# Kernel optimization log

Measured on AMD Instinct MI355X. Metric: run time of the kernel, lower is better.

The kernel has to match this reference:

```python
import jax, jax.numpy as jnp
import numpy as np

B, S, E = 4, 2048, 512
H, D = 8, 64
MIN_W, MAX_W = 256, 1024
EPS = 1e-6


def setup_inputs() -> dict:
    key = jax.random.key(0)
    ks = jax.random.split(key, 9)
    w = lambda k, shp: jax.random.normal(k, shp, dtype=jnp.float32) * 0.02
    return {
        "x": jax.random.normal(ks[0], (B, S, E), dtype=jnp.float32),
        "rms1_w": jnp.ones((E,), jnp.float32),
        "rms2_w": jnp.ones((E,), jnp.float32),
        "qkv_w": w(ks[1], (3 * E, E)),
        "out_w": w(ks[2], (E, E)),
        "cs_w1": w(ks[3], (E // 4, E)),
        "cs_w2": w(ks[4], (1, E // 4)),
        "gate_w": w(ks[5], (2304, E)),
        "up_w": w(ks[6], (2304, E)),
        "down_w": w(ks[7], (E, 2304)),
    }


def _rmsnorm(x, w):
    rms = jax.lax.rsqrt(jnp.mean(x * x, axis=-1, keepdims=True) + EPS)
    return x * rms * w


def _rotate_half(x):
    x1 = x[..., ::2]
    x2 = x[..., 1::2]
    return jnp.stack((-x2, x1), axis=-1).reshape(x.shape)


def reference(x, rms1_w, rms2_w, qkv_w, out_w, cs_w1, cs_w2, gate_w, up_w, down_w):
    # --- pre-norm ---
    h = _rmsnorm(x, rms1_w)                                  # [B,S,E]
    # --- qkv ---
    qkv = h @ qkv_w.T                                        # [B,S,3E]
    qkv = qkv.reshape(B, S, 3, H, D).transpose(2, 0, 3, 1, 4)
    q, k, v = qkv[0], qkv[1], qkv[2]                         # [B,H,S,D]
    # --- RoPE (cat-freqs cos/sin + interleaved rotate_half, as in source) ---
    inv_freq = 1.0 / (10000.0 ** (jnp.arange(0, D, 2, dtype=jnp.float32) / D))
    pos = jnp.arange(S, dtype=jnp.float32)
    freqs = jnp.outer(pos, inv_freq)                         # [S,D/2]
    emb = jnp.concatenate([freqs, freqs], axis=-1)           # [S,D]
    cos = jnp.cos(emb)[None, None]
    sin = jnp.sin(emb)[None, None]
    q = q * cos + _rotate_half(q) * sin
    k = k * cos + _rotate_half(k) * sin
    # --- attention scores ---
    scale = D ** -0.5
    scores = jnp.einsum("bhqd,bhkd->bhqk", q, k) * scale     # [B,H,S,S]
    # --- complexity -> dynamic window size ---
    n = S * E
    mu = jnp.mean(h, axis=(1, 2), keepdims=True)
    var = jnp.sum((h - mu) ** 2, axis=(1, 2)) / (n - 1)      # unbiased, per batch
    var_norm = jax.nn.sigmoid(var * 10.0 - 5.0)
    xm = jnp.mean(h, axis=1)                                 # [B,E]
    learned = jax.nn.sigmoid((jax.nn.silu(xm @ cs_w1.T)) @ cs_w2.T)[:, 0]
    complexity = (var_norm + learned) / 2.0                  # [B]
    ws_f = MIN_W + jnp.mean(complexity) * (MAX_W - MIN_W)
    ws = ws_f.astype(jnp.int32)                              # trunc, like .int()
    ws = jnp.maximum(jnp.minimum(ws, S), MIN_W)
    # --- causal + sliding-window mask ---
    p = jnp.arange(S)
    rel = p[:, None] - p[None, :]                            # [S,S]
    allowed = (rel >= 0) & (rel < ws)
    scores = jnp.where(allowed[None, None], scores, -jnp.inf)
    attn = jax.nn.softmax(scores, axis=-1)
    out = jnp.einsum("bhqk,bhkd->bhqd", attn, v)             # [B,H,S,D]
    out = out.transpose(0, 2, 1, 3).reshape(B, S, E)
    out = out @ out_w.T
    x = x + out
    # --- SwiGLU FFN ---
    h2 = _rmsnorm(x, rms2_w)
    ffn = (jax.nn.silu(h2 @ gate_w.T) * (h2 @ up_w.T)) @ down_w.T
    return x + ffn
```

## Files before the change

### kernel.cpp

```cpp
#include <hip/hip_runtime.h>

typedef unsigned short u16;
typedef unsigned int   u32;
typedef __attribute__((ext_vector_type(4))) float  f32x4;
typedef __attribute__((ext_vector_type(8))) __bf16 bf16x8;
typedef __attribute__((ext_vector_type(4))) u32    u32x4;
typedef __attribute__((ext_vector_type(2))) u32    u32x2;

#define B_ 4
#define S_ 2048
#define E_ 512
#define H_ 8
#define D_ 64

__device__ __forceinline__ u16 f2bf(float f) {
  union { float f; u32 u; } a; a.f = f;
  u32 r = a.u + 0x7FFFu + ((a.u >> 16) & 1u);
  return (u16)(r >> 16);
}
__device__ __forceinline__ float bf2f(u16 u) {
  union { u32 u; float f; } a; a.u = (u32)u << 16;
  return a.f;
}
__device__ __forceinline__ u32 pkbf(float lo, float hi) {
  u32 r;
  asm("v_cvt_pk_bf16_f32 %0, %1, %2" : "=v"(r) : "v"(lo), "v"(hi));
  return r;
}

#define GLOAD16(gp, lp) __builtin_amdgcn_global_load_lds( \
    (const __attribute__((address_space(1))) void*)(gp),  \
    (__attribute__((address_space(3))) void*)(lp), 16, 0, 0)

#define BARRIER() asm volatile("s_barrier" ::: "memory")

__global__ __launch_bounds__(256) void prep_k(const float* __restrict__ qkv_w,
                                              const float* __restrict__ out_w,
                                              const float* __restrict__ gate_w,
                                              const float* __restrict__ up_w,
                                              const float* __restrict__ down_w,
                                              u16* __restrict__ wqkv, u16* __restrict__ wout,
                                              u16* __restrict__ wgate, u16* __restrict__ wup,
                                              u16* __restrict__ wdown,
                                              float* __restrict__ ct, float* __restrict__ st) {
  int bid = (int)blockIdx.x;
  const float* s; u16* d; int base;
  if (bid < 768)       { s = qkv_w;  d = wqkv;  base = bid; }
  else if (bid < 1024) { s = out_w;  d = wout;  base = bid - 768; }
  else if (bid < 2176) { s = gate_w; d = wgate; base = bid - 1024; }
  else if (bid < 3328) { s = up_w;   d = wup;   base = bid - 2176; }
  else if (bid < 4480) { s = down_w; d = wdown; base = bid - 3328; }
  else {
    int idx = (bid - 4480) * 256 + threadIdx.x;
    int sp = idx >> 6, j = idx & 63;
    float f = powf(10000.f, -(float)(j & 31) * (1.f / 32.f));
    float ang = (float)sp * f;
    ct[idx] = cosf(ang);
    st[idx] = sinf(ang);
    return;
  }
  int i = (base * 256 + threadIdx.x) * 4;
  f32x4 v = *(const f32x4*)(s + i);
  u32x2 o;
  o.x = pkbf(v[0], v[1]);
  o.y = pkbf(v[2], v[3]);
  *(u32x2*)(d + i) = o;
}

__global__ __launch_bounds__(256) void rmsnorm_k(const float* __restrict__ x,
                                                 const float* __restrict__ wv,
                                                 u16* __restrict__ o) {
  const int row = blockIdx.x;
  const int t = threadIdx.x;
  const float* xr = x + (size_t)row * E_;
  float v0 = xr[t], v1 = xr[t + 256];
  float ss = v0 * v0 + v1 * v1;
#pragma unroll
  for (int m = 1; m < 64; m <<= 1) ss += __shfl_xor(ss, m, 64);
  __shared__ float red[4];
  if ((t & 63) == 0) red[t >> 6] = ss;
  __syncthreads();
  float tot = red[0] + red[1] + red[2] + red[3];
  float rms = 1.f / sqrtf(tot * (1.f / (float)E_) + 1e-6f);
  o[(size_t)row * E_ + t]       = f2bf(v0 * rms * wv[t]);
  o[(size_t)row * E_ + t + 256] = f2bf(v1 * rms * wv[t + 256]);
}

__global__ __launch_bounds__(256) void colsum_k(const u16* __restrict__ h,
                                                float* __restrict__ st) {
  const int b = blockIdx.x >> 3, ck = blockIdx.x & 7;
  const u16* hb = h + ((size_t)b * S_ + ck * 256) * E_;
  const int t = threadIdx.x;
  float a0 = 0, a1 = 0, s = 0, sq = 0;
  for (int r = 0; r < 256; ++r) {
    float v0 = bf2f(hb[(size_t)r * E_ + t]);
    float v1 = bf2f(hb[(size_t)r * E_ + t + 256]);
    a0 += v0; a1 += v1;
    s += v0 + v1; sq += v0 * v0 + v1 * v1;
  }
  atomicAdd(&st[8 + b * E_ + t], a0);
  atomicAdd(&st[8 + b * E_ + t + 256], a1);
#pragma unroll
  for (int m = 1; m < 64; m <<= 1) { s += __shfl_xor(s, m, 64); sq += __shfl_xor(sq, m, 64); }
  if ((t & 63) == 0) { atomicAdd(&st[b], s); atomicAdd(&st[4 + b], sq); }
}

__global__ __launch_bounds__(128) void wscalc_k(float* __restrict__ st,
                                                const float* __restrict__ w1,
                                                const float* __restrict__ w2) {
  const int j = threadIdx.x;
  __shared__ float comp[4];
  __shared__ float tw[2];
  float dot[4] = {0.f, 0.f, 0.f, 0.f};
  const float* w1r = w1 + (size_t)j * E_;
  for (int e = 0; e < E_; ++e) {
    float wv = w1r[e];
    dot[0] += st[8 + 0 * E_ + e] * wv;
    dot[1] += st[8 + 1 * E_ + e] * wv;
    dot[2] += st[8 + 2 * E_ + e] * wv;
    dot[3] += st[8 + 3 * E_ + e] * wv;
  }
  for (int b = 0; b < 4; ++b) {
    float d = dot[b] * (1.f / (float)S_);
    float si = d / (1.f + __expf(-d));
    float term = si * w2[j];
#pragma unroll
    for (int m = 1; m < 64; m <<= 1) term += __shfl_xor(term, m, 64);
    __syncthreads();
    if ((j & 63) == 0) tw[j >> 6] = term;
    __syncthreads();
    if (j == 0) {
      float pre = tw[0] + tw[1];
      float learned = 1.f / (1.f + __expf(-pre));
      const float n = (float)S_ * (float)E_;
      float sum = st[b], ssq = st[4 + b];
      float var = (ssq - sum * sum / n) / (n - 1.f);
      float vn = 1.f / (1.f + __expf(-(var * 10.f - 5.f)));
      comp[b] = 0.5f * (vn + learned);
    }
    __syncthreads();
  }
  if (j == 0) {
    float mean = 0.25f * (comp[0] + comp[1] + comp[2] + comp[3]);
    float wsf = 256.f + mean * 768.f;
    int v = (int)wsf;
    v = v < 256 ? 256 : (v > S_ ? S_ : v);
    ((int*)st)[2056] = v;
  }
}

struct EpiArgs {
  u16* q; u16* k; u16* vt;
  const float* cosT; const float* sinT;
  const float* resid; float* outf;
};

template <int N, int K, int EPI>
__global__ __launch_bounds__(512) void gemm_k(const u16* __restrict__ A,
                                              const u16* __restrict__ W,
                                              EpiArgs ea) {
  constexpr int NBN = N / 128;
  __shared__ u16 sA[2][128 * 64];
  __shared__ u16 sB[2][128 * 64];
  const int tid = threadIdx.x;
  const int nwg = (int)gridDim.x;
  const int bid = (int)blockIdx.x;
  const int logical = (bid & 7) * (nwg >> 3) + (bid >> 3);
  const int bm = logical / NBN, bn = logical % NBN;
  const int lane = tid & 63, w = tid >> 6;
  const int g = lane >> 4, c = lane & 15;
  const int wrow = (w >> 1) * 32;
  const int wcol = (w & 1) * 64;

  const int lr0 = lane >> 3;
  const int scol = ((lane & 7) ^ lr0) * 8;
  const u16* gA = A + (size_t)(bm * 128 + w * 16 + lr0) * K + scol;
  const u16* gB = W + (size_t)(bn * 128 + w * 16 + lr0) * K + scol;

  f32x4 acc[2][4];
  f32x4 zz = {0.f, 0.f, 0.f, 0.f};
#pragma unroll
  for (int i = 0; i < 2; ++i)
#pragma unroll
    for (int j = 0; j < 4; ++j) acc[i][j] = zz;

  auto stage = [&](int buf, int ko) {
    GLOAD16(gA + ko,                (char*)sA[buf] + (w * 16) * 128);
    GLOAD16(gA + (size_t)8 * K + ko, (char*)sA[buf] + (w * 16 + 8) * 128);
    GLOAD16(gB + ko,                (char*)sB[buf] + (w * 16) * 128);
    GLOAD16(gB + (size_t)8 * K + ko, (char*)sB[buf] + (w * 16 + 8) * 128);
  };

  constexpr int NIT = K / 64;
  stage(0, 0);
  int cur = 0;
  for (int it = 0; it < NIT; ++it) {
    if (it + 1 < NIT) {
      stage(cur ^ 1, (it + 1) * 64);
      asm volatile("s_waitcnt vmcnt(4)" ::: "memory");
    } else {
      asm volatile("s_waitcnt vmcnt(0)" ::: "memory");
    }
    BARRIER();
    const u16* bufA = sA[cur];
    const u16* bufB = sB[cur];
    bf16x8 af[2][2], bfr[4][2];
#pragma unroll
    for (int mi = 0; mi < 2; ++mi) {
      int ar = wrow + mi * 16 + c;
#pragma unroll
      for (int kk = 0; kk < 2; ++kk)
        af[mi][kk] = *(const bf16x8*)&bufA[ar * 64 + (((kk * 4 + g) ^ (ar & 7)) * 8)];
    }
#pragma unroll
    for (int nj = 0; nj < 4; ++nj) {
      int br = wcol + nj * 16 + c;
#pragma unroll
      for (int kk = 0; kk < 2; ++kk)
        bfr[nj][kk] = *(const bf16x8*)&bufB[br * 64 + (((kk * 4 + g) ^ (br & 7)) * 8)];
    }
#pragma unroll
    for (int kk = 0; kk < 2; ++kk)
#pragma unroll
      for (int mi = 0; mi < 2; ++mi)
#pragma unroll
        for (int nj = 0; nj < 4; ++nj)
          acc[mi][nj] = __builtin_amdgcn_mfma_f32_16x16x32_bf16(af[mi][kk], bfr[nj][kk], acc[mi][nj], 0, 0, 0);
    BARRIER();
    cur ^= 1;
  }

#pragma unroll
  for (int mi = 0; mi < 2; ++mi) {
#pragma unroll
    for (int nj = 0; nj < 4; ++nj) {
      const int rowb = bm * 128 + wrow + mi * 16 + 4 * g;
      const int cc = bn * 128 + wcol + nj * 16 + c;
      if constexpr (EPI == 0) {
        const int which = cc >> 9;
        const int hh = (cc >> 6) & 7;
        const int d = cc & 63;
        const int bi = rowb >> 11;
        const int s = rowb & (S_ - 1);
        if (which == 2) {
          u32x2 pk;
          pk.x = pkbf(acc[mi][nj][0], acc[mi][nj][1]);
          pk.y = pkbf(acc[mi][nj][2], acc[mi][nj][3]);
          *(u32x2*)(ea.vt + (((size_t)(bi * H_ + hh) * D_ + d) * S_ + s)) = pk;
        } else {
          u16* dst = (which == 0 ? ea.q : ea.k) + (((size_t)(bi * H_ + hh) * S_ + s) * D_ + d);
#pragma unroll
          for (int r = 0; r < 4; ++r) {
            float v = acc[mi][nj][r];
            float pv = __shfl_xor(v, 1, 64);
            int si = s + r;
            float cs = ea.cosT[si * 64 + d];
            float sn = ea.sinT[si * 64 + d];
            float o = v * cs + ((d & 1) ? pv : -pv) * sn;
            dst[(size_t)r * D_] = f2bf(o);
          }
        }
      } else {
#pragma unroll
        for (int r = 0; r < 4; ++r) {
          size_t idx = (size_t)(rowb + r) * N + cc;
          ea.outf[idx] = acc[mi][nj][r] + ea.resid[idx];
        }
      }
    }
  }
}

__global__ __launch_bounds__(512) void gemmgu_k(const u16* __restrict__ A,
                                                const u16* __restrict__ Wg,
                                                const u16* __restrict__ Wu,
                                                u16* __restrict__ outb) {
  __shared__ u16 sA[2][128 * 32];
  __shared__ u16 sG[2][128 * 32];
  __shared__ u16 sU[2][128 * 32];
  const int tid = threadIdx.x;
  const int nwg = (int)gridDim.x;
  const int bid = (int)blockIdx.x;
  const int logical = (bid & 7) * (nwg >> 3) + (bid >> 3);
  const int bm = logical / 18, bn = logical % 18;
  const int lane = tid & 63, w = tid >> 6;
  const int g = lane >> 4, c = lane & 15;
  const int wrow = (w >> 1) * 32;
  const int wcol = (w & 1) * 64;

  const int sr0 = w * 16 + (lane >> 2);
  const int ch0 = (lane & 3) ^ ((sr0 >> 1) & 3);
  const u16* gA = A + (size_t)(bm * 128 + sr0) * 512 + ch0 * 8;
  const u16* gG = Wg + (size_t)(bn * 128 + sr0) * 512 + ch0 * 8;
  const u16* gU = Wu + (size_t)(bn * 128 + sr0) * 512 + ch0 * 8;
  const int lofs = w * 1024;

  f32x4 accg[2][4], accu[2][4];
  f32x4 zz = {0.f, 0.f, 0.f, 0.f};
#pragma unroll
  for (int i = 0; i < 2; ++i)
#pragma unroll
    for (int j = 0; j < 4; ++j) { accg[i][j] = zz; accu[i][j] = zz; }

  auto stage = [&](int buf, int ko) {
    GLOAD16(gA + ko, (char*)sA[buf] + lofs);
    GLOAD16(gG + ko, (char*)sG[buf] + lofs);
    GLOAD16(gU + ko, (char*)sU[buf] + lofs);
  };

  stage(0, 0);
  int cur = 0;
  for (int it = 0; it < 16; ++it) {
    if (it + 1 < 16) {
      stage(cur ^ 1, (it + 1) * 32);
      asm volatile("s_waitcnt vmcnt(3)" ::: "memory");
    } else {
      asm volatile("s_waitcnt vmcnt(0)" ::: "memory");
    }
    BARRIER();
    const u16* bufA = sA[cur];
    const u16* bufG = sG[cur];
    const u16* bufU = sU[cur];
    bf16x8 af[2], bg[4], bu[4];
#pragma unroll
    for (int mi = 0; mi < 2; ++mi) {
      int ar = wrow + mi * 16 + c;
      af[mi] = *(const bf16x8*)&bufA[ar * 32 + ((g ^ ((ar >> 1) & 3)) * 8)];
    }
#pragma unroll
    for (int nj = 0; nj < 4; ++nj) {
      int br = wcol + nj * 16 + c;
      int sw = (g ^ ((br >> 1) & 3)) * 8;
      bg[nj] = *(const bf16x8*)&bufG[br * 32 + sw];
      bu[nj] = *(const bf16x8*)&bufU[br * 32 + sw];
    }
#pragma unroll
    for (int mi = 0; mi < 2; ++mi)
#pragma unroll
      for (int nj = 0; nj < 4; ++nj) {
        accg[mi][nj] = __builtin_amdgcn_mfma_f32_16x16x32_bf16(af[mi], bg[nj], accg[mi][nj], 0, 0, 0);
        accu[mi][nj] = __builtin_amdgcn_mfma_f32_16x16x32_bf16(af[mi], bu[nj], accu[mi][nj], 0, 0, 0);
      }
    BARRIER();
    cur ^= 1;
  }

#pragma unroll
  for (int mi = 0; mi < 2; ++mi) {
#pragma unroll
    for (int nj = 0; nj < 4; ++nj) {
      const int rowb = bm * 128 + wrow + mi * 16 + 4 * g;
      const int cc = bn * 128 + wcol + nj * 16 + c;
#pragma unroll
      for (int r = 0; r < 4; ++r) {
        float gv = accg[mi][nj][r];
        float uv = accu[mi][nj][r];
        float sil = gv / (1.f + __expf(-gv));
        outb[(size_t)(rowb + r) * 2304 + cc] = f2bf(sil * uv);
      }
    }
  }
}

__global__ __launch_bounds__(256) void attn_k(const u16* __restrict__ Qb,
                                              const u16* __restrict__ Kb,
                                              const u16* __restrict__ Vt,
                                              u16* __restrict__ ao,
                                              const int* __restrict__ wsp) {
  __shared__ u16 sK[2][64 * 64];
  __shared__ u16 sV[2][64 * 64];
  const int bid = (int)blockIdx.x;
  const int qt = 31 - (bid >> 5);
  const int bh = bid & 31;
  const int b = bh >> 3, h = bh & 7;
  const int tid = threadIdx.x;
  const int w = tid >> 6, lane = tid & 63;
  const int g = lane >> 4, c = lane & 15;
  const int ws = *wsp;
  const int qw = qt * 64 + w * 16;
  const u16* Qh = Qb + (size_t)bh * S_ * D_;
  const u16* Kh = Kb + (size_t)bh * S_ * D_;
  const u16* Vh = Vt + (size_t)bh * D_ * S_;

  bf16x8 qf0 = *(const bf16x8*)(Qh + (qw + c) * D_ + g * 8);
  bf16x8 qf1 = *(const bf16x8*)(Qh + (qw + c) * D_ + 32 + g * 8);

  const int lr0 = lane >> 3;
  const int scol = ((lane & 7) ^ lr0) * 8;
  const u16* gK = Kh + (size_t)(w * 16 + lr0) * D_ + scol;
  const u16* gV = Vh + (size_t)(w * 16 + lr0) * S_ + scol;

  const float SCL = 0.125f * 1.44269504089f;
  float m2 = -3e38f, lsum = 0.f;
  f32x4 O[4];
  f32x4 zz = {0.f, 0.f, 0.f, 0.f};
#pragma unroll
  for (int i = 0; i < 4; ++i) O[i] = zz;

  int lo_w = qw - ws + 1;
  if (lo_w < 0) lo_w = 0;
  int lo_blk = qt * 64 - ws + 1;
  if (lo_blk < 0) lo_blk = 0;
  lo_blk &= ~63;
  const int qhi = qt * 64 + 63;
  const int nkb = (qhi - lo_blk) / 64 + 1;
  const int q = qw + c;

  auto stageKV = [&](int buf, int kb) {
    GLOAD16(gK + (size_t)kb * D_,            (char*)sK[buf] + (w * 16) * 128);
    GLOAD16(gK + (size_t)(kb + 8) * D_,      (char*)sK[buf] + (w * 16 + 8) * 128);
    GLOAD16(gV + kb,                         (char*)sV[buf] + (w * 16) * 128);
    GLOAD16(gV + kb + (size_t)8 * S_,        (char*)sV[buf] + (w * 16 + 8) * 128);
  };

  stageKV(0, lo_blk);
  asm volatile("s_waitcnt vmcnt(0)" ::: "memory");
  BARRIER();
  int cur = 0;
  for (int i = 0; i < nkb; ++i) {
    const int kb = lo_blk + i * 64;
    if (i + 1 < nkb) stageKV(cur ^ 1, kb + 64);
    if (kb <= qw + 15 && kb + 63 >= lo_w) {
      const u16* bK = sK[cur];
      const u16* bV = sV[cur];
      f32x4 st4[4];
      __builtin_amdgcn_s_setprio(1);
#pragma unroll
      for (int t = 0; t < 4; ++t) {
        const int kr = 16 * t + c;
        bf16x8 k0 = *(const bf16x8*)&bK[kr * 64 + ((g ^ (kr & 7)) * 8)];
        bf16x8 k1 = *(const bf16x8*)&bK[kr * 64 + (((4 + g) ^ (kr & 7)) * 8)];
        f32x4 s = zz;
        s = __builtin_amdgcn_mfma_f32_16x16x32_bf16(k0, qf0, s, 0, 0, 0);
        s = __builtin_amdgcn_mfma_f32_16x16x32_bf16(k1, qf1, s, 0, 0, 0);
        st4[t] = s;
      }
      __builtin_amdgcn_s_setprio(0);
      const bool interior = (kb + 63 <= qw) && (kb >= qw + 16 - ws);
      float p[4][4];
      float bm = -3e38f;
      if (interior) {
#pragma unroll
        for (int t = 0; t < 4; ++t)
#pragma unroll
          for (int r = 0; r < 4; ++r) {
            p[t][r] = st4[t][r] * SCL;
            bm = fmaxf(bm, p[t][r]);
          }
      } else {
#pragma unroll
        for (int t = 0; t < 4; ++t)
#pragma unroll
          for (int r = 0; r < 4; ++r) {
            int ki = kb + 16 * t + 4 * g + r;
            float v = st4[t][r] * SCL;
            bool ok = (q >= ki) && (q - ki) < ws;
            p[t][r] = ok ? v : -__builtin_inff();
            bm = fmaxf(bm, p[t][r]);
          }
      }
      bm = fmaxf(bm, __shfl_xor(bm, 16, 64));
      bm = fmaxf(bm, __shfl_xor(bm, 32, 64));
      if (!__all(bm - m2 <= 8.f)) {
        float mnew = fmaxf(m2, bm);
        float al = exp2f(m2 - mnew);
        lsum *= al;
#pragma unroll
        for (int ii = 0; ii < 4; ++ii) O[ii] *= al;
        m2 = mnew;
      }
      float psum = 0.f;
#pragma unroll
      for (int t = 0; t < 4; ++t)
#pragma unroll
        for (int r = 0; r < 4; ++r) {
          p[t][r] = exp2f(p[t][r] - m2);
          psum += p[t][r];
        }
      psum += __shfl_xor(psum, 16, 64);
      psum += __shfl_xor(psum, 32, 64);
      lsum += psum;

      u32 pp[4][2];
#pragma unroll
      for (int t = 0; t < 4; ++t) {
        pp[t][0] = pkbf(p[t][0], p[t][1]);
        pp[t][1] = pkbf(p[t][2], p[t][3]);
      }
      const int lA = (g & 1) * 32 + c;
      const int lB = lA + 16;
      const int hi = g >> 1;
      union { bf16x8 v; u32 u[4]; } pf0, pf1;
#pragma unroll
      for (int wi = 0; wi < 2; ++wi) {
        u32 a0 = (u32)__shfl((int)pp[0][wi], lA, 64);
        u32 a1 = (u32)__shfl((int)pp[1][wi], lA, 64);
        u32 a2 = (u32)__shfl((int)pp[2][wi], lA, 64);
        u32 a3 = (u32)__shfl((int)pp[3][wi], lA, 64);
        u32 b0 = (u32)__shfl((int)pp[0][wi], lB, 64);
        u32 b1 = (u32)__shfl((int)pp[1][wi], lB, 64);
        u32 b2 = (u32)__shfl((int)pp[2][wi], lB, 64);
        u32 b3 = (u32)__shfl((int)pp[3][wi], lB, 64);
        pf0.u[wi]     = hi ? a1 : a0;
        pf0.u[2 + wi] = hi ? b1 : b0;
        pf1.u[wi]     = hi ? a3 : a2;
        pf1.u[2 + wi] = hi ? b3 : b2;
      }
      __builtin_amdgcn_s_setprio(1);
#pragma unroll
      for (int dt = 0; dt < 4; ++dt) {
        const int vr = dt * 16 + c;
        bf16x8 v0 = *(const bf16x8*)&bV[vr * 64 + ((g ^ (vr & 7)) * 8)];
        bf16x8 v1 = *(const bf16x8*)&bV[vr * 64 + (((4 + g) ^ (vr & 7)) * 8)];
        O[dt] = __builtin_amdgcn_mfma_f32_16x16x32_bf16(v0, pf0.v, O[dt], 0, 0, 0);
        O[dt] = __builtin_amdgcn_mfma_f32_16x16x32_bf16(v1, pf1.v, O[dt], 0, 0, 0);
      }
      __builtin_amdgcn_s_setprio(0);
    }
    asm volatile("s_waitcnt vmcnt(0)" ::: "memory");
    BARRIER();
    cur ^= 1;
  }

  const float inv = 1.f / lsum;
  u16* orow = ao + ((size_t)(b * S_ + qw + c)) * E_ + h * D_;
#pragma unroll
  for (int dt = 0; dt < 4; ++dt) {
    u32x2 pk;
    pk.x = pkbf(O[dt][0] * inv, O[dt][1] * inv);
    pk.y = pkbf(O[dt][2] * inv, O[dt][3] * inv);
    *(u32x2*)(orow + dt * 16 + 4 * g) = pk;
  }
}

extern "C" void kernel_launch(void* const* d_in, const int* in_sizes, int n_in,
                              void* d_out, int out_size, void* d_ws, size_t ws_size,
                              hipStream_t stream) {
  const float* x      = (const float*)d_in[0];
  const float* rms1_w = (const float*)d_in[1];
  const float* rms2_w = (const float*)d_in[2];
  const float* qkv_w  = (const float*)d_in[3];
  const float* out_w  = (const float*)d_in[4];
  const float* cs_w1  = (const float*)d_in[5];
  const float* cs_w2  = (const float*)d_in[6];
  const float* gate_w = (const float*)d_in[7];
  const float* up_w   = (const float*)d_in[8];
  const float* down_w = (const float*)d_in[9];

  char* ws = (char*)d_ws;
  constexpr size_t o_wqkv = 0;
  constexpr size_t o_wout = 1572864;
  constexpr size_t o_wgate = 2097152;
  constexpr size_t o_wup = 4456448;
  constexpr size_t o_wdown = 6815744;
  constexpr size_t o_h = 9175040;
  constexpr size_t o_stats = 17563648;
  constexpr size_t o_cos = 17580032;
  constexpr size_t o_sin = 18104320;
  constexpr size_t o_Q = 18628608;
  constexpr size_t o_K = 27017216;
  constexpr size_t o_Vt = 35405824;
  constexpr size_t o_x2 = 43794432;
  constexpr size_t o_gate = 60571648;

  u16* wqkv = (u16*)(ws + o_wqkv);
  u16* wout = (u16*)(ws + o_wout);
  u16* wgate = (u16*)(ws + o_wgate);
  u16* wup = (u16*)(ws + o_wup);
  u16* wdown = (u16*)(ws + o_wdown);
  u16* h = (u16*)(ws + o_h);
  float* stats = (float*)(ws + o_stats);
  float* cosT = (float*)(ws + o_cos);
  float* sinT = (float*)(ws + o_sin);
  u16* Qb = (u16*)(ws + o_Q);
  u16* Kb = (u16*)(ws + o_K);
  u16* Vt = (u16*)(ws + o_Vt);
  float* x2 = (float*)(ws + o_x2);
  u16* gateb = (u16*)(ws + o_gate);
  u16* attno = h;
  u16* h2 = Qb;

  hipMemsetAsync(stats, 0, 16384, stream);
  prep_k<<<4992, 256, 0, stream>>>(qkv_w, out_w, gate_w, up_w, down_w,
                                   wqkv, wout, wgate, wup, wdown, cosT, sinT);

  rmsnorm_k<<<8192, 256, 0, stream>>>(x, rms1_w, h);
  colsum_k<<<32, 256, 0, stream>>>(h, stats);
  wscalc_k<<<1, 128, 0, stream>>>(stats, cs_w1, cs_w2);

  EpiArgs ea{};
  ea.q = Qb; ea.k = Kb; ea.vt = Vt; ea.cosT = cosT; ea.sinT = sinT;
  gemm_k<1536, 512, 0><<<768, 512, 0, stream>>>(h, wqkv, ea);

  attn_k<<<1024, 256, 0, stream>>>(Qb, Kb, Vt, attno, (const int*)(stats + 2056));

  EpiArgs e2{};
  e2.resid = x; e2.outf = x2;
  gemm_k<512, 512, 1><<<256, 512, 0, stream>>>(attno, wout, e2);

  rmsnorm_k<<<8192, 256, 0, stream>>>(x2, rms2_w, h2);

  gemmgu_k<<<1152, 512, 0, stream>>>(h2, wgate, wup, gateb);

  EpiArgs e5{};
  e5.resid = x2; e5.outf = (float*)d_out;
  gemm_k<512, 2304, 1><<<256, 512, 0, stream>>>(gateb, wdown, e5);

  (void)in_sizes; (void)n_in; (void)out_size; (void)ws_size;
}
```

Before: 326.5 us.

## Triple-buffer generic GEMM with BK=32 and widen gate/up GEMM tile to 256 rows

The generic GEMM kernel moves from a double-buffered BK=64 pipeline to a triple-buffered BK=32 pipeline. It prefetches two stages ahead and needs a single barrier per iteration. The fused gate/up GEMM now computes a 256x128 output tile per workgroup, with 4x4 accumulators per wave for each of gate and up. This halves the grid and reuses each staged gate/up weight fragment across twice as many rows. The costs are more accumulator registers and possibly lower occupancy, plus twice as many K iterations in the generic GEMM.

```diff
diff --git a/kernel.cpp b/kernel.cpp
--- a/kernel.cpp
+++ b/kernel.cpp
@@ -160,8 +160,9 @@
                                               const u16* __restrict__ W,
                                               EpiArgs ea) {
   constexpr int NBN = N / 128;
-  __shared__ u16 sA[2][128 * 64];
-  __shared__ u16 sB[2][128 * 64];
+  constexpr int NIT = K / 32;
+  __shared__ u16 sA[3][128 * 32];
+  __shared__ u16 sB[3][128 * 32];
   const int tid = threadIdx.x;
   const int nwg = (int)gridDim.x;
   const int bid = (int)blockIdx.x;
@@ -172,10 +173,11 @@
   const int wrow = (w >> 1) * 32;
   const int wcol = (w & 1) * 64;
 
-  const int lr0 = lane >> 3;
-  const int scol = ((lane & 7) ^ lr0) * 8;
-  const u16* gA = A + (size_t)(bm * 128 + w * 16 + lr0) * K + scol;
-  const u16* gB = W + (size_t)(bn * 128 + w * 16 + lr0) * K + scol;
+  const int srow = tid >> 2;
+  const int sch = (tid & 3) ^ ((srow >> 1) & 3);
+  const u16* gA = A + (size_t)(bm * 128 + srow) * K + sch * 8;
+  const u16* gB = W + (size_t)(bn * 128 + srow) * K + sch * 8;
+  const int lofs = w * 1024;
 
   f32x4 acc[2][4];
   f32x4 zz = {0.f, 0.f, 0.f, 0.f};
@@ -185,49 +187,43 @@
     for (int j = 0; j < 4; ++j) acc[i][j] = zz;
 
   auto stage = [&](int buf, int ko) {
-    GLOAD16(gA + ko,                (char*)sA[buf] + (w * 16) * 128);
-    GLOAD16(gA + (size_t)8 * K + ko, (char*)sA[buf] + (w * 16 + 8) * 128);
-    GLOAD16(gB + ko,                (char*)sB[buf] + (w * 16) * 128);
-    GLOAD16(gB + (size_t)8 * K + ko, (char*)sB[buf] + (w * 16 + 8) * 128);
+    GLOAD16(gA + ko, (char*)sA[buf] + lofs);
+    GLOAD16(gB + ko, (char*)sB[buf] + lofs);
   };
 
-  constexpr int NIT = K / 64;
   stage(0, 0);
-  int cur = 0;
+  stage(1, 32);
+  int rb = 0;
   for (int it = 0; it < NIT; ++it) {
-    if (it + 1 < NIT) {
-      stage(cur ^ 1, (it + 1) * 64);
+    BARRIER();
+    if (it + 2 < NIT) {
+      int sb = (rb == 0) ? 2 : rb - 1;
+      stage(sb, (it + 2) * 32);
       asm volatile("s_waitcnt vmcnt(4)" ::: "memory");
+    } else if (it + 1 < NIT) {
+      asm volatile("s_waitcnt vmcnt(2)" ::: "memory");
     } else {
       asm volatile("s_waitcnt vmcnt(0)" ::: "memory");
     }
-    BARRIER();
-    const u16* bufA = sA[cur];
-    const u16* bufB = sB[cur];
-    bf16x8 af[2][2], bfr[4][2];
+    const u16* bufA = sA[rb];
+    const u16* bufB = sB[rb];
+    bf16x8 af[2], bfr[4];
 #pragma unroll
     for (int mi = 0; mi < 2; ++mi) {
       int ar = wrow + mi * 16 + c;
-#pragma unroll
-      for (int kk = 0; kk < 2; ++kk)
-        af[mi][kk] = *(const bf16x8*)&bufA[ar * 64 + (((kk * 4 + g) ^ (ar & 7)) * 8)];
+      af[mi] = *(const bf16x8*)&bufA[ar * 32 + ((g ^ ((ar >> 1) & 3)) * 8)];
     }
 #pragma unroll
     for (int nj = 0; nj < 4; ++nj) {
       int br = wcol + nj * 16 + c;
-#pragma unroll
-      for (int kk = 0; kk < 2; ++kk)
-        bfr[nj][kk] = *(const bf16x8*)&bufB[br * 64 + (((kk * 4 + g) ^ (br & 7)) * 8)];
-    }
-#pragma unroll
-    for (int kk = 0; kk < 2; ++kk)
-#pragma unroll
-      for (int mi = 0; mi < 2; ++mi)
-#pragma unroll
-        for (int nj = 0; nj < 4; ++nj)
-          acc[mi][nj] = __builtin_amdgcn_mfma_f32_16x16x32_bf16(af[mi][kk], bfr[nj][kk], acc[mi][nj], 0, 0, 0);
-    BARRIER();
-    cur ^= 1;
+      bfr[nj] = *(const bf16x8*)&bufB[br * 32 + ((g ^ ((br >> 1) & 3)) * 8)];
+    }
+#pragma unroll
+    for (int mi = 0; mi < 2; ++mi)
+#pragma unroll
+      for (int nj = 0; nj < 4; ++nj)
+        acc[mi][nj] = __builtin_amdgcn_mfma_f32_16x16x32_bf16(af[mi], bfr[nj], acc[mi][nj], 0, 0, 0);
+    rb = (rb == 2) ? 0 : rb + 1;
   }
 
 #pragma unroll
@@ -275,7 +271,7 @@
                                                 const u16* __restrict__ Wg,
                                                 const u16* __restrict__ Wu,
                                                 u16* __restrict__ outb) {
-  __shared__ u16 sA[2][128 * 32];
+  __shared__ u16 sA[2][256 * 32];
   __shared__ u16 sG[2][128 * 32];
   __shared__ u16 sU[2][128 * 32];
   const int tid = threadIdx.x;
@@ -285,27 +281,29 @@
   const int bm = logical / 18, bn = logical % 18;
   const int lane = tid & 63, w = tid >> 6;
   const int g = lane >> 4, c = lane & 15;
-  const int wrow = (w >> 1) * 32;
+  const int wrow = (w >> 1) * 64;
   const int wcol = (w & 1) * 64;
 
-  const int sr0 = w * 16 + (lane >> 2);
-  const int ch0 = (lane & 3) ^ ((sr0 >> 1) & 3);
-  const u16* gA = A + (size_t)(bm * 128 + sr0) * 512 + ch0 * 8;
-  const u16* gG = Wg + (size_t)(bn * 128 + sr0) * 512 + ch0 * 8;
-  const u16* gU = Wu + (size_t)(bn * 128 + sr0) * 512 + ch0 * 8;
+  const int srow = tid >> 2;
+  const int sch = (tid & 3) ^ ((srow >> 1) & 3);
+  const u16* gA  = A + (size_t)(bm * 256 + srow) * 512 + sch * 8;
+  const u16* gA2 = A + (size_t)(bm * 256 + 128 + srow) * 512 + sch * 8;
+  const u16* gG  = Wg + (size_t)(bn * 128 + srow) * 512 + sch * 8;
+  const u16* gU  = Wu + (size_t)(bn * 128 + srow) * 512 + sch * 8;
   const int lofs = w * 1024;
 
-  f32x4 accg[2][4], accu[2][4];
+  f32x4 accg[4][4], accu[4][4];
   f32x4 zz = {0.f, 0.f, 0.f, 0.f};
 #pragma unroll
-  for (int i = 0; i < 2; ++i)
+  for (int i = 0; i < 4; ++i)
 #pragma unroll
     for (int j = 0; j < 4; ++j) { accg[i][j] = zz; accu[i][j] = zz; }
 
   auto stage = [&](int buf, int ko) {
-    GLOAD16(gA + ko, (char*)sA[buf] + lofs);
-    GLOAD16(gG + ko, (char*)sG[buf] + lofs);
-    GLOAD16(gU + ko, (char*)sU[buf] + lofs);
+    GLOAD16(gA + ko,  (char*)sA[buf] + lofs);
+    GLOAD16(gA2 + ko, (char*)sA[buf] + 8192 + lofs);
+    GLOAD16(gG + ko,  (char*)sG[buf] + lofs);
+    GLOAD16(gU + ko,  (char*)sU[buf] + lofs);
   };
 
   stage(0, 0);
@@ -313,7 +311,7 @@
   for (int it = 0; it < 16; ++it) {
     if (it + 1 < 16) {
       stage(cur ^ 1, (it + 1) * 32);
-      asm volatile("s_waitcnt vmcnt(3)" ::: "memory");
+      asm volatile("s_waitcnt vmcnt(4)" ::: "memory");
     } else {
       asm volatile("s_waitcnt vmcnt(0)" ::: "memory");
     }
@@ -321,9 +319,9 @@
     const u16* bufA = sA[cur];
     const u16* bufG = sG[cur];
     const u16* bufU = sU[cur];
-    bf16x8 af[2], bg[4], bu[4];
-#pragma unroll
-    for (int mi = 0; mi < 2; ++mi) {
+    bf16x8 af[4];
+#pragma unroll
+    for (int mi = 0; mi < 4; ++mi) {
       int ar = wrow + mi * 16 + c;
       af[mi] = *(const bf16x8*)&bufA[ar * 32 + ((g ^ ((ar >> 1) & 3)) * 8)];
     }
@@ -331,25 +329,23 @@
     for (int nj = 0; nj < 4; ++nj) {
       int br = wcol + nj * 16 + c;
       int sw = (g ^ ((br >> 1) & 3)) * 8;
-      bg[nj] = *(const bf16x8*)&bufG[br * 32 + sw];
-      bu[nj] = *(const bf16x8*)&bufU[br * 32 + sw];
-    }
-#pragma unroll
-    for (int mi = 0; mi < 2; ++mi)
-#pragma unroll
-      for (int nj = 0; nj < 4; ++nj) {
-        accg[mi][nj] = __builtin_amdgcn_mfma_f32_16x16x32_bf16(af[mi], bg[nj], accg[mi][nj], 0, 0, 0);
-        accu[mi][nj] = __builtin_amdgcn_mfma_f32_16x16x32_bf16(af[mi], bu[nj], accu[mi][nj], 0, 0, 0);
-      }
+      bf16x8 bg = *(const bf16x8*)&bufG[br * 32 + sw];
+      bf16x8 bu = *(const bf16x8*)&bufU[br * 32 + sw];
+#pragma unroll
+      for (int mi = 0; mi < 4; ++mi) {
+        accg[mi][nj] = __builtin_amdgcn_mfma_f32_16x16x32_bf16(af[mi], bg, accg[mi][nj], 0, 0, 0);
+        accu[mi][nj] = __builtin_amdgcn_mfma_f32_16x16x32_bf16(af[mi], bu, accu[mi][nj], 0, 0, 0);
+      }
+    }
     BARRIER();
     cur ^= 1;
   }
 
 #pragma unroll
-  for (int mi = 0; mi < 2; ++mi) {
+  for (int mi = 0; mi < 4; ++mi) {
 #pragma unroll
     for (int nj = 0; nj < 4; ++nj) {
-      const int rowb = bm * 128 + wrow + mi * 16 + 4 * g;
+      const int rowb = bm * 256 + wrow + mi * 16 + 4 * g;
       const int cc = bn * 128 + wcol + nj * 16 + c;
 #pragma unroll
       for (int r = 0; r < 4; ++r) {
@@ -407,10 +403,10 @@
   const int q = qw + c;
 
   auto stageKV = [&](int buf, int kb) {
-    GLOAD16(gK + (size_t)kb * D_,            (char*)sK[buf] + (w * 16) * 128);
-    GLOAD16(gK + (size_t)(kb + 8) * D_,      (char*)sK[buf] + (w * 16 + 8) * 128);
-    GLOAD16(gV + kb,                         (char*)sV[buf] + (w * 16) * 128);
-    GLOAD16(gV + kb + (size_t)8 * S_,        (char*)sV[buf] + (w * 16 + 8) * 128);
+    GLOAD16(gK + (size_t)kb * D_,       (char*)sK[buf] + (w * 16) * 128);
+    GLOAD16(gK + (size_t)(kb + 8) * D_, (char*)sK[buf] + (w * 16 + 8) * 128);
+    GLOAD16(gV + kb,                    (char*)sV[buf] + (w * 16) * 128);
+    GLOAD16(gV + kb + (size_t)8 * S_,   (char*)sV[buf] + (w * 16 + 8) * 128);
   };
 
   stageKV(0, lo_blk);
@@ -600,7 +596,7 @@
 
   rmsnorm_k<<<8192, 256, 0, stream>>>(x2, rms2_w, h2);
 
-  gemmgu_k<<<1152, 512, 0, stream>>>(h2, wgate, wup, gateb);
+  gemmgu_k<<<576, 512, 0, stream>>>(h2, wgate, wup, gateb);
 
   EpiArgs e5{};
   e5.resid = x2; e5.outf = (float*)d_out;
```

After: 336.7 us. +3.1%, slower.
